# Kernel optimization log

Measured on AMD Instinct MI355X. Metric: run time of the kernel, lower is better.

Reference implementation:

```python
import jax, jax.numpy as jnp
import numpy as np

B, C_IN, N = 64, 64, 4097          # N = T + 1 (index 0 is the null node)
T = N - 1
HID, LAT = 128, 64
EPS = 1e-5


def _tree_conv(trees, children, W, b):
    # trees: (B, C, N); children: (B, 3T) int indices into node axis
    Bn, C, _ = trees.shape
    idx = jnp.broadcast_to(children[:, None, :], (Bn, C, children.shape[1]))
    g = jnp.take_along_axis(trees, idx, axis=2)        # (B, C, 3T) gather
    g = g.reshape(Bn, C, -1, 3)                        # (B, C, T, 3)
    out = jnp.einsum('bctk,ock->bot', g, W) + b[None, :, None]  # (B, O, T)
    zero = jnp.zeros((Bn, out.shape[1], 1), out.dtype)  # null-node column
    return jnp.concatenate([zero, out], axis=2)         # (B, O, T+1)


def _tree_layer_norm(x):
    # normalize over (channels, nodes) per example; torch.std -> ddof=1
    mean = jnp.mean(x, axis=(1, 2), keepdims=True)
    std = jnp.std(x, axis=(1, 2), ddof=1, keepdims=True)
    return (x - mean) / (std + EPS)


def _encode(feats, children, W1, b1, W2, b2):
    x = _tree_conv(feats, children, W1, b1)
    x = jax.nn.relu(_tree_layer_norm(x))
    x = _tree_conv(x, children, W2, b2)
    x = jax.nn.relu(_tree_layer_norm(x))   # dropout is identity in eval
    return jnp.max(x, axis=2)              # DynamicPooling: (B, HID)


def setup_inputs() -> dict:
    key = jax.random.key(0)
    ks = jax.random.split(key, 12)
    s_in = 1.0 / np.sqrt(3 * C_IN)
    s_h = 1.0 / np.sqrt(3 * HID)
    s_fc = 1.0 / np.sqrt(2 * HID)
    return {
        'logical_feats': jax.random.normal(ks[0], (B, C_IN, N), jnp.float32),
        'physical_feats': jax.random.normal(ks[1], (B, C_IN, N), jnp.float32),
        'children': jax.random.randint(ks[2], (B, 3 * T), 0, N, jnp.int32),
        'Wl1': jax.random.normal(ks[3], (HID, C_IN, 3), jnp.float32) * s_in,
        'bl1': jnp.zeros((HID,), jnp.float32),
        'Wl2': jax.random.normal(ks[4], (HID, HID, 3), jnp.float32) * s_h,
        'bl2': jnp.zeros((HID,), jnp.float32),
        'Wp1': jax.random.normal(ks[5], (HID, C_IN, 3), jnp.float32) * s_in,
        'bp1': jnp.zeros((HID,), jnp.float32),
        'Wp2': jax.random.normal(ks[6], (HID, HID, 3), jnp.float32) * s_h,
        'bp2': jnp.zeros((HID,), jnp.float32),
        'Wmu': jax.random.normal(ks[7], (LAT, 2 * HID), jnp.float32) * s_fc,
        'bmu': jnp.zeros((LAT,), jnp.float32),
        'Wlv': jax.random.normal(ks[8], (LAT, 2 * HID), jnp.float32) * s_fc,
        'blv': jnp.zeros((LAT,), jnp.float32),
    }


def reference(logical_feats, physical_feats, children,
              Wl1, bl1, Wl2, bl2, Wp1, bp1, Wp2, bp2,
              Wmu, bmu, Wlv, blv):
    # NOTE: source module passes log_children to BOTH encoders; kept faithful.
    l_embed = _encode(logical_feats, children, Wl1, bl1, Wl2, bl2)
    p_embed = _encode(physical_feats, children, Wp1, bp1, Wp2, bp2)
    combined = jnp.concatenate([l_embed, p_embed], axis=-1)  # (B, 2*HID)
    mu = combined @ Wmu.T + bmu
    logvar = combined @ Wlv.T + blv
    return mu, logvar
```

## Files before the change

### kernel.cpp

```cpp
#include <hip/hip_runtime.h>
#include <hip/hip_bf16.h>

#define NODES 4097
#define TT 4096
#define CIN 64
#define HID 128
#define BATCH 64
#define EPS 1e-5f

typedef short bf16x8 __attribute__((ext_vector_type(8)));
typedef float f32x16 __attribute__((ext_vector_type(16)));

__global__ __launch_bounds__(256) void k_transpose(const float* __restrict__ in,
                                                   __hip_bfloat16* __restrict__ out) {
    __shared__ float tile[32][33];
    int b = blockIdx.z;
    int n0 = blockIdx.x * 32;
    int c0 = blockIdx.y * 32;
    int tx = threadIdx.x, ty = threadIdx.y;
    for (int i = 0; i < 32; i += 8) {
        int n = n0 + tx, c = c0 + ty + i;
        float v = 0.f;
        if (n < NODES) v = in[((size_t)b * CIN + c) * NODES + n];
        tile[ty + i][tx] = v;
    }
    __syncthreads();
    for (int i = 0; i < 32; i += 8) {
        int n = n0 + ty + i, c = c0 + tx;
        if (n < NODES) out[((size_t)b * NODES + n) * CIN + c] = __float2bfloat16(tile[tx][ty + i]);
    }
}

__global__ void k_wprep(const float* __restrict__ W, __hip_bfloat16* __restrict__ Wp, int C) {
    int id = blockIdx.x * 256 + threadIdx.x;
    int total = 3 * C * HID / 8;
    if (id >= total) return;
    int lane = id & 63;
    int ct = (id >> 6) & 3;
    int ks = id >> 8;
    int n = ct * 32 + (lane & 31);
    int kb = ks * 16 + (lane >> 5) * 8;
    union { int4 i; __hip_bfloat16 h[8]; } u;
#pragma unroll
    for (int j = 0; j < 8; ++j) {
        int k = kb + j;
        int slot = k / C, c = k % C;
        u.h[j] = __float2bfloat16(W[(n * C + c) * 3 + slot]);
    }
    ((int4*)Wp)[id] = u.i;
}

template <int C, bool NORM, bool POOL>
__global__ __launch_bounds__(256) void k_conv_mfma(
    const __hip_bfloat16* __restrict__ xTb,
    const int* __restrict__ children,
    const __hip_bfloat16* __restrict__ Wp,
    const float* __restrict__ bias,
    const float* __restrict__ ms,
    __hip_bfloat16* __restrict__ y,
    float* __restrict__ sums,
    float* __restrict__ pool_part) {
    constexpr int KSc = C / 16;
    constexpr int CH8 = C / 8;
    const int b = blockIdx.y;
    const int t0 = blockIdx.x * 128;
    const int tid = threadIdx.x;
    const int lane = tid & 63;
    const int w = tid >> 6;
    const int rg2 = w >> 1;
    const int ct2 = w & 1;

    __shared__ __align__(16) ushort A_lds[4 * KSc * 65 * 8];

    float mean = 0.f, scale = 1.f;
    if (NORM) { mean = ms[b * 2]; scale = ms[b * 2 + 1]; }

    f32x16 acc[2][2] = {};

    const long cbase = (long)b * (3 * TT) + (long)t0 * 3;
    const int4* WpB = (const int4*)Wp;

    for (int slot = 0; slot < 3; ++slot) {
        if (slot) __syncthreads();
#pragma unroll
        for (int it = 0; it < (128 * CH8) / 256; ++it) {
            int idx = it * 256 + tid;
            int t = idx / CH8;
            int c8 = idx % CH8;
            int child = children[cbase + t * 3 + slot];
            union { int4 i; __hip_bfloat16 h[8]; } u;
            u.i = *(const int4*)(xTb + ((size_t)b * NODES + child) * C + c8 * 8);
            if (NORM) {
#pragma unroll
                for (int j = 0; j < 8; ++j) {
                    float f = __bfloat162float(u.h[j]);
                    f = (f - mean) * scale;
                    u.h[j] = __float2bfloat16(f > 0.f ? f : 0.f);
                }
            }
            int ks = c8 >> 1, half = c8 & 1;
            int idx16 = ((t >> 5) * KSc + ks) * 65 + (t & 31) + 32 * half;
            ((int4*)A_lds)[idx16] = u.i;
        }
        __syncthreads();

#pragma unroll
        for (int ks = 0; ks < KSc; ++ks) {
            int ksg = slot * KSc + ks;
            bf16x8 a0 = *(const bf16x8*)&A_lds[(((2 * rg2 + 0) * KSc + ks) * 65 + lane) * 8];
            bf16x8 a1 = *(const bf16x8*)&A_lds[(((2 * rg2 + 1) * KSc + ks) * 65 + lane) * 8];
            union { int4 i; bf16x8 v; } b0, b1;
            b0.i = WpB[(ksg * 4 + 2 * ct2 + 0) * 64 + lane];
            b1.i = WpB[(ksg * 4 + 2 * ct2 + 1) * 64 + lane];
            acc[0][0] = __builtin_amdgcn_mfma_f32_32x32x16_bf16(a0, b0.v, acc[0][0], 0, 0, 0);
            acc[0][1] = __builtin_amdgcn_mfma_f32_32x32x16_bf16(a0, b1.v, acc[0][1], 0, 0, 0);
            acc[1][0] = __builtin_amdgcn_mfma_f32_32x32x16_bf16(a1, b0.v, acc[1][0], 0, 0, 0);
            acc[1][1] = __builtin_amdgcn_mfma_f32_32x32x16_bf16(a1, b1.v, acc[1][1], 0, 0, 0);
        }
    }

    float bsum = 0.f, bss = 0.f;
    float lmax[2] = {-3.4e38f, -3.4e38f};
#pragma unroll
    for (int rgi = 0; rgi < 2; ++rgi) {
#pragma unroll
        for (int cti = 0; cti < 2; ++cti) {
            int o = 64 * ct2 + 32 * cti + (lane & 31);
            float bv = bias[o];
            int rbase = t0 + 64 * rg2 + 32 * rgi + 4 * (lane >> 5) + 1;
            f32x16 a = acc[rgi][cti];
#pragma unroll
            for (int reg = 0; reg < 16; ++reg) {
                float v = a[reg] + bv;
                bsum += v;
                bss += v * v;
                if (POOL) {
                    lmax[cti] = fmaxf(lmax[cti], v);
                } else {
                    int row = rbase + (reg & 3) + 8 * (reg >> 2);
                    y[((size_t)b * NODES + row) * HID + o] = __float2bfloat16(v);
                }
            }
        }
    }
    if (!POOL && blockIdx.x == 0 && tid < HID)
        y[(size_t)b * NODES * HID + tid] = __float2bfloat16(0.f);

    __syncthreads();
    float* red = (float*)A_lds;
    float* pm = red + 512;
    red[tid] = bsum;
    red[256 + tid] = bss;
    if (POOL) {
        int slice = 2 * rg2 + (lane >> 5);
        pm[(64 * ct2 + (lane & 31)) * 4 + slice] = lmax[0];
        pm[(64 * ct2 + 32 + (lane & 31)) * 4 + slice] = lmax[1];
    }
    __syncthreads();
    for (int s = 128; s > 0; s >>= 1) {
        if (tid < s) { red[tid] += red[tid + s]; red[256 + tid] += red[256 + tid + s]; }
        __syncthreads();
    }
    if (tid == 0) {
        atomicAdd(&sums[b * 2], red[0]);
        atomicAdd(&sums[b * 2 + 1], red[256]);
    }
    if (POOL && tid < HID) {
        float m = fmaxf(fmaxf(pm[tid * 4], pm[tid * 4 + 1]),
                        fmaxf(pm[tid * 4 + 2], pm[tid * 4 + 3]));
        pool_part[((size_t)b * 32 + blockIdx.x) * HID + tid] = m;
    }
}

__global__ void k_stats(const float* __restrict__ sums, float* __restrict__ ms) {
    int b = threadIdx.x;
    const float M = (float)HID * (float)NODES;
    float S = sums[b * 2], SS = sums[b * 2 + 1];
    float mean = S / M;
    float var = (SS - S * S / M) / (M - 1.f);
    float sd = sqrtf(fmaxf(var, 0.f));
    ms[b * 2] = mean;
    ms[b * 2 + 1] = 1.f / (sd + EPS);
}

__global__ __launch_bounds__(128) void k_pool_fin(const float* __restrict__ part,
                                                  const float* __restrict__ ms,
                                                  float* __restrict__ combined, int enc_off) {
    int b = blockIdx.x;
    int o = threadIdx.x;
    float m = 0.f;
#pragma unroll 4
    for (int s = 0; s < 32; ++s)
        m = fmaxf(m, part[((size_t)b * 32 + s) * HID + o]);
    float v = (m - ms[b * 2]) * ms[b * 2 + 1];
    combined[b * 2 * HID + enc_off + o] = v > 0.f ? v : 0.f;
}

__global__ __launch_bounds__(128) void k_fc(const float* __restrict__ combined,
                                            const float* __restrict__ Wmu, const float* __restrict__ bmu,
                                            const float* __restrict__ Wlv, const float* __restrict__ blv,
                                            float* __restrict__ out) {
    int b = blockIdx.x;
    int tid = threadIdx.x;
    __shared__ float cb[256];
    cb[tid] = combined[b * 256 + tid];
    cb[tid + 128] = combined[b * 256 + tid + 128];
    __syncthreads();
    const float* W = (tid < 64) ? Wmu : Wlv;
    int l = tid & 63;
    float s = (tid < 64) ? bmu[l] : blv[l];
    for (int j = 0; j < 256; ++j) s += cb[j] * W[l * 256 + j];
    out[(tid < 64 ? 0 : BATCH * 64) + b * 64 + l] = s;
}

extern "C" void kernel_launch(void* const* d_in, const int* in_sizes, int n_in,
                              void* d_out, int out_size, void* d_ws, size_t ws_size,
                              hipStream_t stream) {
    const int* children = (const int*)d_in[2];
    const float* Wmu = (const float*)d_in[11];
    const float* bmu = (const float*)d_in[12];
    const float* Wlv = (const float*)d_in[13];
    const float* blv = (const float*)d_in[14];

    char* ws = (char*)d_ws;
    size_t off = 0;
    auto alloc = [&](size_t bytes) { void* p = ws + off; off += (bytes + 255) & ~(size_t)255; return p; };
    float* sums = (float*)alloc(2 * 2 * BATCH * 2 * sizeof(float));
    float* msbuf = (float*)alloc(2 * 2 * BATCH * 2 * sizeof(float));
    float* combined = (float*)alloc((size_t)BATCH * 256 * sizeof(float));
    float* pool_part = (float*)alloc((size_t)BATCH * 32 * HID * sizeof(float));
    __hip_bfloat16* Wp1 = (__hip_bfloat16*)alloc((size_t)3 * CIN * HID * sizeof(__hip_bfloat16));
    __hip_bfloat16* Wp2 = (__hip_bfloat16*)alloc((size_t)3 * HID * HID * sizeof(__hip_bfloat16));
    __hip_bfloat16* fT = (__hip_bfloat16*)alloc((size_t)BATCH * NODES * CIN * sizeof(__hip_bfloat16));
    __hip_bfloat16* y1 = (__hip_bfloat16*)alloc((size_t)BATCH * NODES * HID * sizeof(__hip_bfloat16));

    hipMemsetAsync(sums, 0, 2 * 2 * BATCH * 2 * sizeof(float), stream);

    for (int enc = 0; enc < 2; ++enc) {
        const float* feats = (const float*)d_in[enc];
        const float* W1 = (const float*)d_in[3 + enc * 4];
        const float* b1 = (const float*)d_in[4 + enc * 4];
        const float* W2 = (const float*)d_in[5 + enc * 4];
        const float* b2 = (const float*)d_in[6 + enc * 4];
        float* sums1 = sums + (enc * 2 + 0) * BATCH * 2;
        float* sums2 = sums + (enc * 2 + 1) * BATCH * 2;
        float* ms1 = msbuf + (enc * 2 + 0) * BATCH * 2;
        float* ms2 = msbuf + (enc * 2 + 1) * BATCH * 2;

        k_transpose<<<dim3((NODES + 31) / 32, CIN / 32, BATCH), dim3(32, 8), 0, stream>>>(feats, fT);
        k_wprep<<<(3 * CIN * HID / 8 + 255) / 256, 256, 0, stream>>>(W1, Wp1, CIN);
        k_wprep<<<(3 * HID * HID / 8 + 255) / 256, 256, 0, stream>>>(W2, Wp2, HID);

        k_conv_mfma<CIN, false, false><<<dim3(TT / 128, BATCH), 256, 0, stream>>>(
            fT, children, Wp1, b1, nullptr, y1, sums1, nullptr);
        k_stats<<<1, BATCH, 0, stream>>>(sums1, ms1);
        k_conv_mfma<HID, true, true><<<dim3(TT / 128, BATCH), 256, 0, stream>>>(
            y1, children, Wp2, b2, ms1, nullptr, sums2, pool_part);
        k_stats<<<1, BATCH, 0, stream>>>(sums2, ms2);
        k_pool_fin<<<BATCH, 128, 0, stream>>>(pool_part, ms2, combined, enc * HID);
    }

    k_fc<<<BATCH, 128, 0, stream>>>(combined, Wmu, bmu, Wlv, blv, (float*)d_out);
}
```

Measured before the change: 449.0 us.

## Batch both encoders per launch, gather via direct global-to-LDS loads, split normalization out

Merges the two encoder passes into single launches by adding an encoder grid dimension, which halves the kernel count and doubles the grid size per launch. The child-row gather now uses global_load_lds to write straight into LDS in the MFMA operand layout, skipping register staging. Because that path cannot transform data in flight, the layer-norm plus ReLU moves out of the second conv into a separate in-place k_norm pass over y1. The cost is an extra full read and write of the intermediate activations, and the workspace doubles to hold both encoders at once.

```diff
diff --git a/kernel.cpp b/kernel.cpp
--- a/kernel.cpp
+++ b/kernel.cpp
@@ -11,10 +11,21 @@
 typedef short bf16x8 __attribute__((ext_vector_type(8)));
 typedef float f32x16 __attribute__((ext_vector_type(16)));
 
-__global__ __launch_bounds__(256) void k_transpose(const float* __restrict__ in,
+__device__ __forceinline__ void load_lds16(const void* g, void* l) {
+    __builtin_amdgcn_global_load_lds(
+        (const __attribute__((address_space(1))) unsigned int*)(uintptr_t)g,
+        (__attribute__((address_space(3))) unsigned int*)(uintptr_t)l,
+        16, 0, 0);
+}
+
+__global__ __launch_bounds__(256) void k_transpose(const float* __restrict__ f0,
+                                                   const float* __restrict__ f1,
                                                    __hip_bfloat16* __restrict__ out) {
     __shared__ float tile[32][33];
-    int b = blockIdx.z;
+    int z = blockIdx.z;
+    int enc = z >> 6, b = z & 63;
+    const float* in = enc ? f1 : f0;
+    __hip_bfloat16* o = out + (size_t)enc * BATCH * NODES * CIN;
     int n0 = blockIdx.x * 32;
     int c0 = blockIdx.y * 32;
     int tx = threadIdx.x, ty = threadIdx.y;
@@ -27,11 +38,15 @@
     __syncthreads();
     for (int i = 0; i < 32; i += 8) {
         int n = n0 + ty + i, c = c0 + tx;
-        if (n < NODES) out[((size_t)b * NODES + n) * CIN + c] = __float2bfloat16(tile[tx][ty + i]);
-    }
-}
-
-__global__ void k_wprep(const float* __restrict__ W, __hip_bfloat16* __restrict__ Wp, int C) {
+        if (n < NODES) o[((size_t)b * NODES + n) * CIN + c] = __float2bfloat16(tile[tx][ty + i]);
+    }
+}
+
+__global__ void k_wprep(const float* __restrict__ W0, const float* __restrict__ W1,
+                        __hip_bfloat16* __restrict__ Wp, int C) {
+    int enc = blockIdx.y;
+    const float* W = enc ? W1 : W0;
+    __hip_bfloat16* o = Wp + (size_t)enc * 3 * C * HID;
     int id = blockIdx.x * 256 + threadIdx.x;
     int total = 3 * C * HID / 8;
     if (id >= total) return;
@@ -47,68 +62,59 @@
         int slot = k / C, c = k % C;
         u.h[j] = __float2bfloat16(W[(n * C + c) * 3 + slot]);
     }
-    ((int4*)Wp)[id] = u.i;
-}
-
-template <int C, bool NORM, bool POOL>
+    ((int4*)o)[id] = u.i;
+}
+
+template <int C, bool POOL>
 __global__ __launch_bounds__(256) void k_conv_mfma(
-    const __hip_bfloat16* __restrict__ xTb,
+    const __hip_bfloat16* __restrict__ xT,
     const int* __restrict__ children,
     const __hip_bfloat16* __restrict__ Wp,
-    const float* __restrict__ bias,
-    const float* __restrict__ ms,
+    const float* __restrict__ bias0, const float* __restrict__ bias1,
     __hip_bfloat16* __restrict__ y,
     float* __restrict__ sums,
     float* __restrict__ pool_part) {
     constexpr int KSc = C / 16;
-    constexpr int CH8 = C / 8;
+    constexpr int TOTK = 3 * KSc;
+    constexpr int NPH = (C == 64) ? 1 : 3;
+    constexpr int PK = TOTK / NPH;
     const int b = blockIdx.y;
+    const int enc = blockIdx.z;
     const int t0 = blockIdx.x * 128;
     const int tid = threadIdx.x;
     const int lane = tid & 63;
     const int w = tid >> 6;
-    const int rg2 = w >> 1;
-    const int ct2 = w & 1;
-
-    __shared__ __align__(16) ushort A_lds[4 * KSc * 65 * 8];
-
-    float mean = 0.f, scale = 1.f;
-    if (NORM) { mean = ms[b * 2]; scale = ms[b * 2 + 1]; }
+    const int rg2 = w >> 1, ct2 = w & 1;
+
+    __shared__ __align__(16) char A_lds[4 * PK * 1024];
+
+    const __hip_bfloat16* x = xT + (size_t)enc * BATCH * NODES * C;
+    const int4* WpB = (const int4*)(Wp + (size_t)enc * 3 * C * HID);
+    const float* bias = enc ? bias1 : bias0;
+    const int sb = enc * BATCH + b;
 
     f32x16 acc[2][2] = {};
-
-    const long cbase = (long)b * (3 * TT) + (long)t0 * 3;
-    const int4* WpB = (const int4*)Wp;
-
-    for (int slot = 0; slot < 3; ++slot) {
-        if (slot) __syncthreads();
-#pragma unroll
-        for (int it = 0; it < (128 * CH8) / 256; ++it) {
-            int idx = it * 256 + tid;
-            int t = idx / CH8;
-            int c8 = idx % CH8;
-            int child = children[cbase + t * 3 + slot];
-            union { int4 i; __hip_bfloat16 h[8]; } u;
-            u.i = *(const int4*)(xTb + ((size_t)b * NODES + child) * C + c8 * 8);
-            if (NORM) {
-#pragma unroll
-                for (int j = 0; j < 8; ++j) {
-                    float f = __bfloat162float(u.h[j]);
-                    f = (f - mean) * scale;
-                    u.h[j] = __float2bfloat16(f > 0.f ? f : 0.f);
-                }
-            }
-            int ks = c8 >> 1, half = c8 & 1;
-            int idx16 = ((t >> 5) * KSc + ks) * 65 + (t & 31) + 32 * half;
-            ((int4*)A_lds)[idx16] = u.i;
+    const size_t rowbase = (size_t)b * NODES;
+    const long cb3 = (long)b * (3 * TT);
+    const int tnode = t0 + w * 32 + (lane & 31);
+
+    for (int ph = 0; ph < NPH; ++ph) {
+        if (ph) __syncthreads();
+#pragma unroll
+        for (int kk = 0; kk < PK; ++kk) {
+            int ksg = ph * PK + kk;
+            int slot = ksg / KSc, ksl = ksg % KSc;
+            int child = children[cb3 + (long)tnode * 3 + slot];
+            const char* g = (const char*)(x + (rowbase + child) * C)
+                          + ksl * 32 + (lane >> 5) * 16;
+            load_lds16(g, A_lds + (w * PK + kk) * 1024);
         }
         __syncthreads();
-
-#pragma unroll
-        for (int ks = 0; ks < KSc; ++ks) {
-            int ksg = slot * KSc + ks;
-            bf16x8 a0 = *(const bf16x8*)&A_lds[(((2 * rg2 + 0) * KSc + ks) * 65 + lane) * 8];
-            bf16x8 a1 = *(const bf16x8*)&A_lds[(((2 * rg2 + 1) * KSc + ks) * 65 + lane) * 8];
+#pragma unroll
+        for (int kk = 0; kk < PK; ++kk) {
+            int ksg = ph * PK + kk;
+            bf16x8 a0 = *(const bf16x8*)(A_lds + ((2 * rg2 + 0) * PK + kk) * 1024 + lane * 16);
+            bf16x8 a1 = *(const bf16x8*)(A_lds + ((2 * rg2 + 1) * PK + kk) * 1024 + lane * 16);
             union { int4 i; bf16x8 v; } b0, b1;
             b0.i = WpB[(ksg * 4 + 2 * ct2 + 0) * 64 + lane];
             b1.i = WpB[(ksg * 4 + 2 * ct2 + 1) * 64 + lane];
@@ -121,6 +127,7 @@
 
     float bsum = 0.f, bss = 0.f;
     float lmax[2] = {-3.4e38f, -3.4e38f};
+    __hip_bfloat16* yp = POOL ? nullptr : (y + (size_t)enc * BATCH * NODES * HID);
 #pragma unroll
     for (int rgi = 0; rgi < 2; ++rgi) {
 #pragma unroll
@@ -138,13 +145,13 @@
                     lmax[cti] = fmaxf(lmax[cti], v);
                 } else {
                     int row = rbase + (reg & 3) + 8 * (reg >> 2);
-                    y[((size_t)b * NODES + row) * HID + o] = __float2bfloat16(v);
+                    yp[(rowbase + row) * HID + o] = __float2bfloat16(v);
                 }
             }
         }
     }
     if (!POOL && blockIdx.x == 0 && tid < HID)
-        y[(size_t)b * NODES * HID + tid] = __float2bfloat16(0.f);
+        yp[rowbase * HID + tid] = __float2bfloat16(0.f);
 
     __syncthreads();
     float* red = (float*)A_lds;
@@ -162,38 +169,56 @@
         __syncthreads();
     }
     if (tid == 0) {
-        atomicAdd(&sums[b * 2], red[0]);
-        atomicAdd(&sums[b * 2 + 1], red[256]);
+        atomicAdd(&sums[sb * 2], red[0]);
+        atomicAdd(&sums[sb * 2 + 1], red[256]);
     }
     if (POOL && tid < HID) {
         float m = fmaxf(fmaxf(pm[tid * 4], pm[tid * 4 + 1]),
                         fmaxf(pm[tid * 4 + 2], pm[tid * 4 + 3]));
-        pool_part[((size_t)b * 32 + blockIdx.x) * HID + tid] = m;
+        pool_part[((size_t)sb * 32 + blockIdx.x) * HID + tid] = m;
     }
 }
 
 __global__ void k_stats(const float* __restrict__ sums, float* __restrict__ ms) {
-    int b = threadIdx.x;
+    int s = threadIdx.x;
     const float M = (float)HID * (float)NODES;
-    float S = sums[b * 2], SS = sums[b * 2 + 1];
+    float S = sums[s * 2], SS = sums[s * 2 + 1];
     float mean = S / M;
     float var = (SS - S * S / M) / (M - 1.f);
     float sd = sqrtf(fmaxf(var, 0.f));
-    ms[b * 2] = mean;
-    ms[b * 2 + 1] = 1.f / (sd + EPS);
+    ms[s * 2] = mean;
+    ms[s * 2 + 1] = 1.f / (sd + EPS);
+}
+
+__global__ __launch_bounds__(256) void k_norm(__hip_bfloat16* __restrict__ y,
+                                              const float* __restrict__ ms) {
+    constexpr int Q = NODES * HID / 8;
+    int s = blockIdx.y;
+    int q = blockIdx.x * 256 + threadIdx.x;
+    if (q >= Q) return;
+    float mean = ms[s * 2], scale = ms[s * 2 + 1];
+    int4* p = (int4*)(y + (size_t)s * NODES * HID) + q;
+    union { int4 i; __hip_bfloat16 h[8]; } u;
+    u.i = *p;
+#pragma unroll
+    for (int j = 0; j < 8; ++j) {
+        float f = (__bfloat162float(u.h[j]) - mean) * scale;
+        u.h[j] = __float2bfloat16(f > 0.f ? f : 0.f);
+    }
+    *p = u.i;
 }
 
 __global__ __launch_bounds__(128) void k_pool_fin(const float* __restrict__ part,
-                                                  const float* __restrict__ ms,
-                                                  float* __restrict__ combined, int enc_off) {
-    int b = blockIdx.x;
-    int o = threadIdx.x;
+                                                  const float* __restrict__ ms1,
+                                                  float* __restrict__ combined) {
+    int b = blockIdx.x, enc = blockIdx.y, o = threadIdx.x;
+    int sb = enc * BATCH + b;
     float m = 0.f;
 #pragma unroll 4
     for (int s = 0; s < 32; ++s)
-        m = fmaxf(m, part[((size_t)b * 32 + s) * HID + o]);
-    float v = (m - ms[b * 2]) * ms[b * 2 + 1];
-    combined[b * 2 * HID + enc_off + o] = v > 0.f ? v : 0.f;
+        m = fmaxf(m, part[((size_t)sb * 32 + s) * HID + o]);
+    float v = (m - ms1[sb * 2]) * ms1[sb * 2 + 1];
+    combined[b * 256 + enc * 128 + o] = v > 0.f ? v : 0.f;
 }
 
 __global__ __launch_bounds__(128) void k_fc(const float* __restrict__ combined,
@@ -228,37 +253,30 @@
     float* sums = (float*)alloc(2 * 2 * BATCH * 2 * sizeof(float));
     float* msbuf = (float*)alloc(2 * 2 * BATCH * 2 * sizeof(float));
     float* combined = (float*)alloc((size_t)BATCH * 256 * sizeof(float));
-    float* pool_part = (float*)alloc((size_t)BATCH * 32 * HID * sizeof(float));
-    __hip_bfloat16* Wp1 = (__hip_bfloat16*)alloc((size_t)3 * CIN * HID * sizeof(__hip_bfloat16));
-    __hip_bfloat16* Wp2 = (__hip_bfloat16*)alloc((size_t)3 * HID * HID * sizeof(__hip_bfloat16));
-    __hip_bfloat16* fT = (__hip_bfloat16*)alloc((size_t)BATCH * NODES * CIN * sizeof(__hip_bfloat16));
-    __hip_bfloat16* y1 = (__hip_bfloat16*)alloc((size_t)BATCH * NODES * HID * sizeof(__hip_bfloat16));
+    float* pool_part = (float*)alloc((size_t)2 * BATCH * 32 * HID * sizeof(float));
+    __hip_bfloat16* Wp1 = (__hip_bfloat16*)alloc((size_t)2 * 3 * CIN * HID * sizeof(__hip_bfloat16));
+    __hip_bfloat16* Wp2 = (__hip_bfloat16*)alloc((size_t)2 * 3 * HID * HID * sizeof(__hip_bfloat16));
+    __hip_bfloat16* fT = (__hip_bfloat16*)alloc((size_t)2 * BATCH * NODES * CIN * sizeof(__hip_bfloat16));
+    __hip_bfloat16* y1 = (__hip_bfloat16*)alloc((size_t)2 * BATCH * NODES * HID * sizeof(__hip_bfloat16));
 
     hipMemsetAsync(sums, 0, 2 * 2 * BATCH * 2 * sizeof(float), stream);
 
-    for (int enc = 0; enc < 2; ++enc) {
-        const float* feats = (const float*)d_in[enc];
-        const float* W1 = (const float*)d_in[3 + enc * 4];
-        const float* b1 = (const float*)d_in[4 + enc * 4];
-        const float* W2 = (const float*)d_in[5 + enc * 4];
-        const float* b2 = (const float*)d_in[6 + enc * 4];
-        float* sums1 = sums + (enc * 2 + 0) * BATCH * 2;
-        float* sums2 = sums + (enc * 2 + 1) * BATCH * 2;
-        float* ms1 = msbuf + (enc * 2 + 0) * BATCH * 2;
-        float* ms2 = msbuf + (enc * 2 + 1) * BATCH * 2;
-
-        k_transpose<<<dim3((NODES + 31) / 32, CIN / 32, BATCH), dim3(32, 8), 0, stream>>>(feats, fT);
-        k_wprep<<<(3 * CIN * HID / 8 + 255) / 256, 256, 0, stream>>>(W1, Wp1, CIN);
-        k_wprep<<<(3 * HID * HID / 8 + 255) / 256, 256, 0, stream>>>(W2, Wp2, HID);
-
-        k_conv_mfma<CIN, false, false><<<dim3(TT / 128, BATCH), 256, 0, stream>>>(
-            fT, children, Wp1, b1, nullptr, y1, sums1, nullptr);
-        k_stats<<<1, BATCH, 0, stream>>>(sums1, ms1);
-        k_conv_mfma<HID, true, true><<<dim3(TT / 128, BATCH), 256, 0, stream>>>(
-            y1, children, Wp2, b2, ms1, nullptr, sums2, pool_part);
-        k_stats<<<1, BATCH, 0, stream>>>(sums2, ms2);
-        k_pool_fin<<<BATCH, 128, 0, stream>>>(pool_part, ms2, combined, enc * HID);
-    }
+    k_wprep<<<dim3(3 * CIN * HID / 8 / 256, 2), 256, 0, stream>>>(
+        (const float*)d_in[3], (const float*)d_in[7], Wp1, CIN);
+    k_wprep<<<dim3(3 * HID * HID / 8 / 256, 2), 256, 0, stream>>>(
+        (const float*)d_in[5], (const float*)d_in[9], Wp2, HID);
+    k_transpose<<<dim3(129, 2, 2 * BATCH), dim3(32, 8), 0, stream>>>(
+        (const float*)d_in[0], (const float*)d_in[1], fT);
+
+    k_conv_mfma<CIN, false><<<dim3(TT / 128, BATCH, 2), 256, 0, stream>>>(
+        fT, children, Wp1, (const float*)d_in[4], (const float*)d_in[8], y1, sums, nullptr);
+    k_stats<<<1, 128, 0, stream>>>(sums, msbuf);
+    k_norm<<<dim3((NODES * HID / 8 + 255) / 256, 2 * BATCH), 256, 0, stream>>>(y1, msbuf);
+    k_conv_mfma<HID, true><<<dim3(TT / 128, BATCH, 2), 256, 0, stream>>>(
+        y1, children, Wp2, (const float*)d_in[6], (const float*)d_in[10], nullptr,
+        sums + 256, pool_part);
+    k_stats<<<1, 128, 0, stream>>>(sums + 256, msbuf + 256);
+    k_pool_fin<<<dim3(BATCH, 2), 128, 0, stream>>>(pool_part, msbuf + 256, combined);
 
     k_fc<<<BATCH, 128, 0, stream>>>(combined, Wmu, bmu, Wlv, blv, (float*)d_out);
 }
```

Result: faster. 438.6 us (-2.3%).
